# Optimization experiments

Measured on AMD Instinct MI355X. Metric: run time of the kernel, lower is better.

Reference implementation:

```python
import jax, jax.numpy as jnp
import numpy as np
from jax import lax

DN = ('NCHW', 'OIHW', 'NCHW')
N_LEVELS = 5


def conv(x, w, b=None, stride=1):
    y = lax.conv_general_dilated(x, w, (stride, stride), 'VALID', dimension_numbers=DN)
    if b is not None:
        y = y + b.reshape(1, -1, 1, 1)
    return y


def conv3_replicate(x, w, b):
    # 3x3 conv, padding=1, padding_mode='replicate'
    xp = jnp.pad(x, ((0, 0), (0, 0), (1, 1), (1, 1)), mode='edge')
    return conv(xp, w, b)


def conv_transpose3_s2(x, w):
    # ConvTranspose2d(k=3, stride=2, padding=0): n -> 2n+1
    return lax.conv_general_dilated(x, jnp.flip(w, (2, 3)), (1, 1), [(2, 2), (2, 2)],
                                    lhs_dilation=(2, 2), dimension_numbers=DN)


def setup_inputs() -> dict:
    key = jax.random.key(0)
    ks = jax.random.split(key, 12)
    B = 1024
    u = jax.random.normal(ks[0], (B, 1, 127, 127), jnp.float32)
    f = jax.random.normal(ks[1], (B, 1, 127, 127), jnp.float32)
    a = jax.random.uniform(ks[2], (B, 1, 128, 128), jnp.float32)
    s = 0.3
    c0_w = jax.random.normal(ks[3], (N_LEVELS, 1, 1, 3, 3), jnp.float32) * s  # Conv_Dyn.conv_0
    c0_b = jax.random.normal(ks[4], (N_LEVELS, 1), jnp.float32) * s
    c1_w = jax.random.normal(ks[5], (N_LEVELS, 1, 1, 2, 2), jnp.float32) * s  # Conv_Dyn.conv_1
    c1_b = jax.random.normal(ks[6], (N_LEVELS, 1), jnp.float32) * s
    r1_w = jax.random.normal(ks[7], (N_LEVELS - 1, 1, 1, 2, 2), jnp.float32) * s  # MgRestriction.R_1
    r3_w = jax.random.normal(ks[8], (N_LEVELS - 1, 1, 1, 3, 3), jnp.float32) * s  # MgRestriction.R_3
    t_w = jax.random.normal(ks[9], (N_LEVELS - 1, 1, 1, 3, 3), jnp.float32) * s  # transpose_layers
    return dict(u=u, f=f, a=a, c0_w=c0_w, c0_b=c0_b, c1_w=c1_w, c1_b=c1_b,
                r1_w=r1_w, r3_w=r3_w, t_w=t_w)


def reference(u, f, a, c0_w, c0_b, c1_w, c1_b, r1_w, r3_w, t_w):
    a_top = a
    # level 0: Conv_Dyn with u given, diva None
    diva = conv(a, c1_w[0], c1_b[0])                 # [B,1,127,127]
    r = f - diva * u
    u_lvl = u + conv3_replicate(jnp.tanh(diva), c0_w[0], c0_b[0]) * r
    diva_list = [diva]
    us = [u_lvl]
    # levels 1..4: restriction then Conv_Dyn (u=None branch, f=None so r kept)
    for i in range(1, N_LEVELS):
        a = conv(a, r1_w[i - 1], stride=2)           # R_1: k2 s2
        r = conv(r, r3_w[i - 1], stride=2)           # R_3: k3 s2
        diva = conv(a, c1_w[i], c1_b[i])
        u_lvl = conv3_replicate(jnp.tanh(diva), c0_w[i], c0_b[i]) * r
        diva_list.append(diva)
        us.append(u_lvl)
    # prolongation: coarse-to-fine residual additions
    for i in range(N_LEVELS - 2, -1, -1):
        us[i] = us[i] + conv_transpose3_s2(us[i + 1], t_w[i])
    return (us[0], f, a_top, *diva_list)
```

## Files before the change

### kernel.cpp

```cpp
#include <hip/hip_runtime.h>
#include <cmath>

#define BATCH 1024

__global__ __launch_bounds__(256, 8) void k_L01(
    const float* __restrict__ u, const float* __restrict__ f, const float* __restrict__ a,
    const float* __restrict__ c0w, const float* __restrict__ c0b,
    const float* __restrict__ c1w, const float* __restrict__ c1b,
    const float* __restrict__ r1w, const float* __restrict__ r3w,
    float* __restrict__ out_us0, float* __restrict__ out_diva0,
    float* __restrict__ out_f, float* __restrict__ out_a,
    float* __restrict__ out_diva1,
    float* __restrict__ ws_a1, float* __restrict__ ws_r1, float* __restrict__ ws_us1)
{
    const int b = blockIdx.y;
    const int bx = blockIdx.x;
    const int Y0 = bx * 8;
    const int y0 = bx * 4;
    const int tid = threadIdx.x;

    __shared__ float asrc[14][128];
    __shared__ float td0[10][128];
    __shared__ float r0s[9][128];
    __shared__ float a1s[7][68];
    __shared__ float td1[6][64];

    {
        const float4* ab4 = reinterpret_cast<const float4*>(a + (size_t)b * 16384);
        float4* s4 = reinterpret_cast<float4*>(&asrc[0][0]);
        const int c4 = tid & 31, r4 = tid >> 5;
        #pragma unroll
        for (int r = r4; r < 14; r += 8) {
            int g = Y0 - 2 + r; g = g < 0 ? 0 : (g > 127 ? 127 : g);
            s4[r * 32 + c4] = ab4[g * 32 + c4];
        }
    }
    __syncthreads();

    const float w00 = c1w[0], w01 = c1w[1], w10 = c1w[2], w11 = c1w[3], b1 = c1b[0];
    const int tx = tid & 127, ty = tid >> 7;

    #pragma unroll
    for (int r = ty; r < 10; r += 2) {
        int g = Y0 - 1 + r;
        if (g >= 0 && g <= 126 && tx < 127) {
            float d = asrc[r + 1][tx] * w00 + asrc[r + 1][tx + 1] * w01
                    + asrc[r + 2][tx] * w10 + asrc[r + 2][tx + 1] * w11 + b1;
            td0[r][tx] = tanhf(d);
        }
    }
    {
        float4* oa4 = reinterpret_cast<float4*>(out_a + (size_t)b * 16384);
        const float4* s4 = reinterpret_cast<const float4*>(&asrc[0][0]);
        const int c4 = tid & 31, r4 = tid >> 5;
        oa4[(Y0 + r4) * 32 + c4] = s4[(r4 + 2) * 32 + c4];
    }
    const float q00 = r1w[0], q01 = r1w[1], q10 = r1w[2], q11 = r1w[3];
    {
        const int tx2 = tid & 63, ty2 = tid >> 6;
        #pragma unroll
        for (int r = ty2; r < 7; r += 4)
            for (int c = tx2; c < 66; c += 64) {
                int ay = y0 - 1 + r; ay = ay < 0 ? 0 : (ay > 63 ? 63 : ay);
                int ax = c - 1; ax = ax < 0 ? 0 : (ax > 63 ? 63 : ax);
                int la = 2 * ay - (Y0 - 2);
                a1s[r][c] = asrc[la][2 * ax] * q00 + asrc[la][2 * ax + 1] * q01
                          + asrc[la + 1][2 * ax] * q10 + asrc[la + 1][2 * ax + 1] * q11;
            }
    }
    __syncthreads();

    const float c0b0 = c0b[0];
    #pragma unroll
    for (int rr = ty; rr < 9; rr += 2) {
        int g = Y0 + rr;
        if (g > 126 || tx >= 127) continue;
        float diva = asrc[rr + 2][tx] * w00 + asrc[rr + 2][tx + 1] * w01
                   + asrc[rr + 3][tx] * w10 + asrc[rr + 3][tx + 1] * w11 + b1;
        size_t idx = (size_t)b * 16129 + (size_t)g * 127 + tx;
        float uv = u[idx], fv = f[idx];
        float rv = fv - diva * uv;
        r0s[rr][tx] = rv;
        if (rr < 8) {
            float s = c0b0;
            #pragma unroll
            for (int ky = 0; ky < 3; ky++) {
                int sy = g - 1 + ky; sy = sy < 0 ? 0 : (sy > 126 ? 126 : sy);
                int lr = sy - (Y0 - 1);
                #pragma unroll
                for (int kx = 0; kx < 3; kx++) {
                    int sx = tx - 1 + kx; sx = sx < 0 ? 0 : (sx > 126 ? 126 : sx);
                    s += c0w[ky * 3 + kx] * td0[lr][sx];
                }
            }
            out_diva0[idx] = diva;
            out_us0[idx] = uv + s * rv;
            out_f[idx] = fv;
        }
    }

    const float v00 = c1w[4], v01 = c1w[5], v10 = c1w[6], v11 = c1w[7], b2 = c1b[1];
    {
        const int tx2 = tid & 63, ty2 = tid >> 6;
        ws_a1[(size_t)b * 4096 + (size_t)(y0 + ty2) * 64 + tx2] = a1s[ty2 + 1][tx2 + 1];
        #pragma unroll
        for (int r = ty2; r < 6; r += 4) {
            int dy = y0 - 1 + r;
            if (dy >= 0 && dy <= 62 && tx2 < 63) {
                float d = a1s[r][tx2 + 1] * v00 + a1s[r][tx2 + 2] * v01
                        + a1s[r + 1][tx2 + 1] * v10 + a1s[r + 1][tx2 + 2] * v11 + b2;
                td1[r][tx2] = tanhf(d);
            }
        }
    }
    __syncthreads();

    {
        const int tx2 = tid & 63, ty2 = tid >> 6;
        const int y = y0 + ty2;
        if (y <= 62 && tx2 < 63) {
            float diva = a1s[ty2 + 1][tx2 + 1] * v00 + a1s[ty2 + 1][tx2 + 2] * v01
                       + a1s[ty2 + 2][tx2 + 1] * v10 + a1s[ty2 + 2][tx2 + 2] * v11 + b2;
            float rv = 0.f;
            #pragma unroll
            for (int p = 0; p < 3; p++)
                #pragma unroll
                for (int q = 0; q < 3; q++)
                    rv += r3w[p * 3 + q] * r0s[2 * ty2 + p][2 * tx2 + q];
            float s = c0b[1];
            #pragma unroll
            for (int ky = 0; ky < 3; ky++) {
                int sy = y - 1 + ky; sy = sy < 0 ? 0 : (sy > 62 ? 62 : sy);
                int lr = sy - (y0 - 1);
                #pragma unroll
                for (int kx = 0; kx < 3; kx++) {
                    int sx = tx2 - 1 + kx; sx = sx < 0 ? 0 : (sx > 62 ? 62 : sx);
                    s += c0w[9 + ky * 3 + kx] * td1[lr][sx];
                }
            }
            size_t idx = (size_t)b * 3969 + (size_t)y * 63 + tx2;
            out_diva1[idx] = diva;
            ws_r1[idx] = rv;
            ws_us1[idx] = s * rv;
        }
    }
}

template<int N, int NA, int PA, int PD>
__device__ __forceinline__ void level_step(
    const float* ap, const float* rp, float* ac, float* rc, float* us, float* td,
    const float* __restrict__ r1w, const float* __restrict__ r3w,
    const float* __restrict__ c1w, float c1b_,
    const float* __restrict__ c0w, float c0b_,
    float* __restrict__ diva_out, int tid)
{
    const float q00 = r1w[0], q01 = r1w[1], q10 = r1w[2], q11 = r1w[3];
    for (int idx = tid; idx < NA * NA; idx += 256) {
        int y = idx / NA, x = idx % NA;
        const float* p = ap + 2 * y * PA + 2 * x;
        ac[idx] = p[0] * q00 + p[1] * q01 + p[PA] * q10 + p[PA + 1] * q11;
    }
    __syncthreads();
    const float w00 = c1w[0], w01 = c1w[1], w10 = c1w[2], w11 = c1w[3];
    for (int idx = tid; idx < N * N; idx += 256) {
        int y = idx / N, x = idx % N;
        float d = ac[y * NA + x] * w00 + ac[y * NA + x + 1] * w01
                + ac[(y + 1) * NA + x] * w10 + ac[(y + 1) * NA + x + 1] * w11 + c1b_;
        td[idx] = tanhf(d);
        diva_out[idx] = d;
    }
    __syncthreads();
    for (int idx = tid; idx < N * N; idx += 256) {
        int y = idx / N, x = idx % N;
        float rv = 0.f;
        #pragma unroll
        for (int p = 0; p < 3; p++)
            #pragma unroll
            for (int q = 0; q < 3; q++)
                rv += r3w[p * 3 + q] * rp[(2 * y + p) * PD + 2 * x + q];
        float s = c0b_;
        #pragma unroll
        for (int ky = 0; ky < 3; ky++) {
            int sy = y - 1 + ky; sy = sy < 0 ? 0 : (sy > N - 1 ? N - 1 : sy);
            #pragma unroll
            for (int kx = 0; kx < 3; kx++) {
                int sx = x - 1 + kx; sx = sx < 0 ? 0 : (sx > N - 1 ? N - 1 : sx);
                s += c0w[ky * 3 + kx] * td[sy * N + sx];
            }
        }
        rc[idx] = rv;
        us[idx] = s * rv;
    }
    __syncthreads();
}

template<int NO, int NI>
__device__ __forceinline__ void prolong_step(
    float* uo, const float* ui, const float* __restrict__ tw9, int tid)
{
    for (int idx = tid; idx < NO * NO; idx += 256) {
        int y = idx / NO, x = idx % NO;
        float acc = 0.f;
        #pragma unroll
        for (int ky = 0; ky < 3; ky++) {
            int sy = y - ky;
            if (sy & 1) continue;
            int iy = sy >> 1;
            if (iy < 0 || iy >= NI) continue;
            #pragma unroll
            for (int kx = 0; kx < 3; kx++) {
                int sx = x - kx;
                if (sx & 1) continue;
                int ix = sx >> 1;
                if (ix < 0 || ix >= NI) continue;
                acc += tw9[ky * 3 + kx] * ui[iy * NI + ix];
            }
        }
        uo[idx] += acc;
    }
    __syncthreads();
}

__global__ __launch_bounds__(256) void k_coarse(
    const float* __restrict__ a1, const float* __restrict__ r1,
    const float* __restrict__ r1w, const float* __restrict__ r3w,
    const float* __restrict__ c1w, const float* __restrict__ c1b,
    const float* __restrict__ c0w, const float* __restrict__ c0b,
    const float* __restrict__ tw,
    float* __restrict__ diva2, float* __restrict__ diva3, float* __restrict__ diva4,
    float* __restrict__ us2_out)
{
    const int b = blockIdx.x;
    const int tid = threadIdx.x;
    __shared__ float aB[32 * 32];
    __shared__ float rB[31 * 31];
    __shared__ float aC[16 * 16];
    __shared__ float rC[15 * 15];
    __shared__ float aD[8 * 8];
    __shared__ float rD[7 * 7];
    __shared__ float us2s[31 * 31];
    __shared__ float us3s[15 * 15];
    __shared__ float us4s[7 * 7];
    __shared__ float td[31 * 31];

    level_step<31, 32, 64, 63>(a1 + (size_t)b * 4096, r1 + (size_t)b * 3969,
        aB, rB, us2s, td,
        r1w + 4, r3w + 9, c1w + 8, c1b[2], c0w + 18, c0b[2],
        diva2 + (size_t)b * 961, tid);
    level_step<15, 16, 32, 31>(aB, rB, aC, rC, us3s, td,
        r1w + 8, r3w + 18, c1w + 12, c1b[3], c0w + 27, c0b[3],
        diva3 + (size_t)b * 225, tid);
    level_step<7, 8, 16, 15>(aC, rC, aD, rD, us4s, td,
        r1w + 12, r3w + 27, c1w + 16, c1b[4], c0w + 36, c0b[4],
        diva4 + (size_t)b * 49, tid);

    prolong_step<15, 7>(us3s, us4s, tw + 27, tid);
    prolong_step<31, 15>(us2s, us3s, tw + 18, tid);

    for (int i = tid; i < 961; i += 256)
        us2_out[(size_t)b * 961 + i] = us2s[i];
}

__global__ __launch_bounds__(256) void k_prolong2(
    float* __restrict__ us0, const float* __restrict__ us1, const float* __restrict__ us2,
    const float* __restrict__ tw)
{
    const int b = blockIdx.y;
    const int bx = blockIdx.x;
    const int Y0 = bx * 16;
    const int y0 = bx * 8;
    const int tid = threadIdx.x;
    __shared__ float us2s[6][32];
    __shared__ float us1p[9][64];

    {
        const float* i2 = us2 + (size_t)b * 961;
        const int tx3 = tid & 31, ty3 = tid >> 5;
        if (ty3 < 6 && tx3 < 31) {
            int jy = 4 * bx - 2 + ty3;
            if (jy >= 0 && jy <= 30) us2s[ty3][tx3] = i2[jy * 31 + tx3];
        }
    }
    __syncthreads();

    const float* t1 = tw + 9;
    {
        const float* i1 = us1 + (size_t)b * 3969;
        const int tx2 = tid & 63, ty2 = tid >> 6;
        #pragma unroll
        for (int r = ty2; r < 9; r += 4) {
            int iy = y0 - 1 + r;
            if (iy < 0 || iy > 62 || tx2 >= 63) continue;
            float acc = i1[iy * 63 + tx2];
            #pragma unroll
            for (int ky = 0; ky < 3; ky++) {
                int sy = iy - ky;
                if ((sy & 1) || sy < 0) continue;
                int jy = sy >> 1;
                if (jy > 30) continue;
                int lr = jy - (4 * bx - 2);
                #pragma unroll
                for (int kx = 0; kx < 3; kx++) {
                    int sx = tx2 - kx;
                    if ((sx & 1) || sx < 0) continue;
                    int jx = sx >> 1;
                    if (jx > 30) continue;
                    acc += t1[ky * 3 + kx] * us2s[lr][jx];
                }
            }
            us1p[r][tx2] = acc;
        }
    }
    __syncthreads();

    const float* t0 = tw;
    {
        float* o0 = us0 + (size_t)b * 16129;
        const int tx = tid & 127, ty = tid >> 7;
        #pragma unroll
        for (int row = ty; row < 16; row += 2) {
            int y = Y0 + row;
            if (y > 126 || tx >= 127) continue;
            float acc = 0.f;
            #pragma unroll
            for (int ky = 0; ky < 3; ky++) {
                int sy = y - ky;
                if ((sy & 1) || sy < 0) continue;
                int iy = sy >> 1;
                if (iy > 62) continue;
                int lr = iy - (y0 - 1);
                #pragma unroll
                for (int kx = 0; kx < 3; kx++) {
                    int sx = tx - kx;
                    if ((sx & 1) || sx < 0) continue;
                    int ix = sx >> 1;
                    if (ix > 62) continue;
                    acc += t0[ky * 3 + kx] * us1p[lr][ix];
                }
            }
            o0[(size_t)y * 127 + tx] += acc;
        }
    }
}

extern "C" void kernel_launch(void* const* d_in, const int* in_sizes, int n_in,
                              void* d_out, int out_size, void* d_ws, size_t ws_size,
                              hipStream_t stream) {
    const float* u   = (const float*)d_in[0];
    const float* f   = (const float*)d_in[1];
    const float* a   = (const float*)d_in[2];
    const float* c0w = (const float*)d_in[3];
    const float* c0b = (const float*)d_in[4];
    const float* c1w = (const float*)d_in[5];
    const float* c1b = (const float*)d_in[6];
    const float* r1w = (const float*)d_in[7];
    const float* r3w = (const float*)d_in[8];
    const float* tw  = (const float*)d_in[9];
    float* out = (float*)d_out;
    float* ws  = (float*)d_ws;
    const size_t B = BATCH;

    size_t off_us0 = 0;
    size_t off_f   = B * 16129;
    size_t off_a   = off_f + B * 16129;
    size_t off_d0  = off_a + B * 16384;
    size_t off_d1  = off_d0 + B * 16129;
    size_t off_d2  = off_d1 + B * 3969;
    size_t off_d3  = off_d2 + B * 961;
    size_t off_d4  = off_d3 + B * 225;

    size_t w_a1  = 0;
    size_t w_r1  = w_a1 + B * 4096;
    size_t w_us1 = w_r1 + B * 3969;
    size_t w_us2 = w_us1 + B * 3969;

    dim3 blk(256);
    k_L01<<<dim3(16, B), blk, 0, stream>>>(
        u, f, a, c0w, c0b, c1w, c1b, r1w, r3w,
        out + off_us0, out + off_d0, out + off_f, out + off_a,
        out + off_d1, ws + w_a1, ws + w_r1, ws + w_us1);

    k_coarse<<<dim3(1024), blk, 0, stream>>>(
        ws + w_a1, ws + w_r1, r1w, r3w, c1w, c1b, c0w, c0b, tw,
        out + off_d2, out + off_d3, out + off_d4, ws + w_us2);

    k_prolong2<<<dim3(8, B), blk, 0, stream>>>(
        out + off_us0, ws + w_us1, ws + w_us2, tw);
}
```

Baseline: 511.0 us.

## Fuse final prolongation into coarse kernel and prefetch u/f before barrier

Removes the separate k_prolong2 launch by having the per-batch k_coarse block compute the level-1 prolongation into a 63x64 shared tile and then add the level-0 transpose-conv contribution directly into us0. This drops the us2 workspace round trip and one kernel launch. In k_L01, the u and f loads move into registers before the first barrier so their latency overlaps the shared-memory fill. The cost is that the final full-resolution pass now runs with only 1024 blocks of 256 threads, each looping over 127 rows, instead of 8192 blocks. It also uses more shared memory and registers in k_coarse, which may reduce parallelism.

```diff
diff --git a/kernel.cpp b/kernel.cpp
--- a/kernel.cpp
+++ b/kernel.cpp
@@ -18,6 +18,7 @@
     const int Y0 = bx * 8;
     const int y0 = bx * 4;
     const int tid = threadIdx.x;
+    const int tx = tid & 127, ty = tid >> 7;
 
     __shared__ float asrc[14][128];
     __shared__ float td0[10][128];
@@ -35,10 +36,22 @@
             s4[r * 32 + c4] = ab4[g * 32 + c4];
         }
     }
+
+    const size_t rowbase = (size_t)b * 16129;
+    float ur[5], fr[5];
+    #pragma unroll
+    for (int k = 0; k < 5; k++) {
+        int rr = ty + 2 * k;
+        int g = Y0 + rr;
+        if (rr < 9 && g <= 126 && tx < 127) {
+            size_t idx = rowbase + (size_t)g * 127 + tx;
+            ur[k] = u[idx];
+            fr[k] = f[idx];
+        }
+    }
     __syncthreads();
 
     const float w00 = c1w[0], w01 = c1w[1], w10 = c1w[2], w11 = c1w[3], b1 = c1b[0];
-    const int tx = tid & 127, ty = tid >> 7;
 
     #pragma unroll
     for (int r = ty; r < 10; r += 2) {
@@ -72,13 +85,15 @@
 
     const float c0b0 = c0b[0];
     #pragma unroll
-    for (int rr = ty; rr < 9; rr += 2) {
+    for (int k = 0; k < 5; k++) {
+        int rr = ty + 2 * k;
+        if (rr >= 9) break;
         int g = Y0 + rr;
         if (g > 126 || tx >= 127) continue;
         float diva = asrc[rr + 2][tx] * w00 + asrc[rr + 2][tx + 1] * w01
                    + asrc[rr + 3][tx] * w10 + asrc[rr + 3][tx + 1] * w11 + b1;
-        size_t idx = (size_t)b * 16129 + (size_t)g * 127 + tx;
-        float uv = u[idx], fv = f[idx];
+        size_t idx = rowbase + (size_t)g * 127 + tx;
+        float uv = ur[k], fv = fr[k];
         float rv = fv - diva * uv;
         r0s[rr][tx] = rv;
         if (rr < 8) {
@@ -223,12 +238,12 @@
 
 __global__ __launch_bounds__(256) void k_coarse(
     const float* __restrict__ a1, const float* __restrict__ r1,
+    const float* __restrict__ us1g, float* __restrict__ us0,
     const float* __restrict__ r1w, const float* __restrict__ r3w,
     const float* __restrict__ c1w, const float* __restrict__ c1b,
     const float* __restrict__ c0w, const float* __restrict__ c0b,
     const float* __restrict__ tw,
-    float* __restrict__ diva2, float* __restrict__ diva3, float* __restrict__ diva4,
-    float* __restrict__ us2_out)
+    float* __restrict__ diva2, float* __restrict__ diva3, float* __restrict__ diva4)
 {
     const int b = blockIdx.x;
     const int tid = threadIdx.x;
@@ -242,6 +257,18 @@
     __shared__ float us3s[15 * 15];
     __shared__ float us4s[7 * 7];
     __shared__ float td[31 * 31];
+    __shared__ float us1p[63 * 64];
+
+    const int cx = tid & 63, ry = tid >> 6;
+    float us1r[16];
+    {
+        const float* u1b = us1g + (size_t)b * 3969;
+        #pragma unroll
+        for (int k = 0; k < 16; k++) {
+            int y = ry + 4 * k;
+            if (y < 63 && cx < 63) us1r[k] = u1b[y * 63 + cx];
+        }
+    }
 
     level_step<31, 32, 64, 63>(a1 + (size_t)b * 4096, r1 + (size_t)b * 3969,
         aB, rB, us2s, td,
@@ -257,88 +284,57 @@
     prolong_step<15, 7>(us3s, us4s, tw + 27, tid);
     prolong_step<31, 15>(us2s, us3s, tw + 18, tid);
 
-    for (int i = tid; i < 961; i += 256)
-        us2_out[(size_t)b * 961 + i] = us2s[i];
-}
-
-__global__ __launch_bounds__(256) void k_prolong2(
-    float* __restrict__ us0, const float* __restrict__ us1, const float* __restrict__ us2,
-    const float* __restrict__ tw)
-{
-    const int b = blockIdx.y;
-    const int bx = blockIdx.x;
-    const int Y0 = bx * 16;
-    const int y0 = bx * 8;
-    const int tid = threadIdx.x;
-    __shared__ float us2s[6][32];
-    __shared__ float us1p[9][64];
-
-    {
-        const float* i2 = us2 + (size_t)b * 961;
-        const int tx3 = tid & 31, ty3 = tid >> 5;
-        if (ty3 < 6 && tx3 < 31) {
-            int jy = 4 * bx - 2 + ty3;
-            if (jy >= 0 && jy <= 30) us2s[ty3][tx3] = i2[jy * 31 + tx3];
-        }
-    }
-    __syncthreads();
-
-    const float* t1 = tw + 9;
-    {
-        const float* i1 = us1 + (size_t)b * 3969;
-        const int tx2 = tid & 63, ty2 = tid >> 6;
-        #pragma unroll
-        for (int r = ty2; r < 9; r += 4) {
-            int iy = y0 - 1 + r;
-            if (iy < 0 || iy > 62 || tx2 >= 63) continue;
-            float acc = i1[iy * 63 + tx2];
-            #pragma unroll
-            for (int ky = 0; ky < 3; ky++) {
-                int sy = iy - ky;
-                if ((sy & 1) || sy < 0) continue;
-                int jy = sy >> 1;
-                if (jy > 30) continue;
-                int lr = jy - (4 * bx - 2);
-                #pragma unroll
-                for (int kx = 0; kx < 3; kx++) {
-                    int sx = tx2 - kx;
-                    if ((sx & 1) || sx < 0) continue;
-                    int jx = sx >> 1;
-                    if (jx > 30) continue;
-                    acc += t1[ky * 3 + kx] * us2s[lr][jx];
-                }
-            }
-            us1p[r][tx2] = acc;
-        }
-    }
-    __syncthreads();
-
-    const float* t0 = tw;
-    {
-        float* o0 = us0 + (size_t)b * 16129;
-        const int tx = tid & 127, ty = tid >> 7;
-        #pragma unroll
-        for (int row = ty; row < 16; row += 2) {
-            int y = Y0 + row;
-            if (y > 126 || tx >= 127) continue;
-            float acc = 0.f;
+    {
+        const float* t1 = tw + 9;
+        #pragma unroll
+        for (int k = 0; k < 16; k++) {
+            int y = ry + 4 * k;
+            if (y >= 63 || cx >= 63) continue;
+            float acc = us1r[k];
             #pragma unroll
             for (int ky = 0; ky < 3; ky++) {
                 int sy = y - ky;
                 if ((sy & 1) || sy < 0) continue;
                 int iy = sy >> 1;
-                if (iy > 62) continue;
-                int lr = iy - (y0 - 1);
+                if (iy > 30) continue;
                 #pragma unroll
                 for (int kx = 0; kx < 3; kx++) {
-                    int sx = tx - kx;
+                    int sx = cx - kx;
                     if ((sx & 1) || sx < 0) continue;
                     int ix = sx >> 1;
-                    if (ix > 62) continue;
-                    acc += t0[ky * 3 + kx] * us1p[lr][ix];
+                    if (ix > 30) continue;
+                    acc += t1[ky * 3 + kx] * us2s[iy * 31 + ix];
                 }
             }
-            o0[(size_t)y * 127 + tx] += acc;
+            us1p[y * 64 + cx] = acc;
+        }
+    }
+    __syncthreads();
+
+    {
+        const float* t0 = tw;
+        const int tx = tid & 127, ty = tid >> 7;
+        float* o0 = us0 + (size_t)b * 16129;
+        if (tx < 127) {
+            for (int y = ty; y < 127; y += 2) {
+                float acc = 0.f;
+                #pragma unroll
+                for (int ky = 0; ky < 3; ky++) {
+                    int sy = y - ky;
+                    if ((sy & 1) || sy < 0) continue;
+                    int iy = sy >> 1;
+                    if (iy > 62) continue;
+                    #pragma unroll
+                    for (int kx = 0; kx < 3; kx++) {
+                        int sx = tx - kx;
+                        if ((sx & 1) || sx < 0) continue;
+                        int ix = sx >> 1;
+                        if (ix > 62) continue;
+                        acc += t0[ky * 3 + kx] * us1p[iy * 64 + ix];
+                    }
+                }
+                o0[(size_t)y * 127 + tx] += acc;
+            }
         }
     }
 }
@@ -372,7 +368,6 @@
     size_t w_a1  = 0;
     size_t w_r1  = w_a1 + B * 4096;
     size_t w_us1 = w_r1 + B * 3969;
-    size_t w_us2 = w_us1 + B * 3969;
 
     dim3 blk(256);
     k_L01<<<dim3(16, B), blk, 0, stream>>>(
@@ -381,9 +376,7 @@
         out + off_d1, ws + w_a1, ws + w_r1, ws + w_us1);
 
     k_coarse<<<dim3(1024), blk, 0, stream>>>(
-        ws + w_a1, ws + w_r1, r1w, r3w, c1w, c1b, c0w, c0b, tw,
-        out + off_d2, out + off_d3, out + off_d4, ws + w_us2);
-
-    k_prolong2<<<dim3(8, B), blk, 0, stream>>>(
-        out + off_us0, ws + w_us1, ws + w_us2, tw);
-}
+        ws + w_a1, ws + w_r1, ws + w_us1, out + off_us0,
+        r1w, r3w, c1w, c1b, c0w, c0b, tw,
+        out + off_d2, out + off_d3, out + off_d4);
+}
```

After: 528.5 us. 1.03x slower.
